# Optimization experiments

Measured on AMD Instinct MI355X. Metric: run time of the kernel, lower is better.

Reference implementation:

```python
import jax, jax.numpy as jnp
import numpy as np

EPS = 1e-06

def _pairwise_giou(pred, target):
    # pred: [B,P,4], target: [B,G,4] -> gious [B,P,G]
    p = pred[:, :, None, :]   # [B,P,1,4]
    t = target[:, None, :, :] # [B,1,G,4]
    pw = jnp.clip(p[..., 2] - p[..., 0] + 1.0, 0.0)
    ph = jnp.clip(p[..., 3] - p[..., 1] + 1.0, 0.0)
    tw = jnp.clip(t[..., 2] - t[..., 0] + 1.0, 0.0)
    th = jnp.clip(t[..., 3] - t[..., 1] + 1.0, 0.0)
    pred_areas = pw * ph
    target_areas = tw * th
    ix1 = jnp.maximum(p[..., 0], t[..., 0])
    iy1 = jnp.maximum(p[..., 1], t[..., 1])
    ix2 = jnp.minimum(p[..., 2], t[..., 2])
    iy2 = jnp.minimum(p[..., 3], t[..., 3])
    iw = jnp.clip(ix2 - ix1 + 1.0, 0.0)
    ih = jnp.clip(iy2 - iy1 + 1.0, 0.0)
    inter = iw * ih
    unions = pred_areas + target_areas - inter
    ious = jnp.maximum(inter / unions, EPS)
    ox1 = jnp.minimum(p[..., 0], t[..., 0])
    oy1 = jnp.minimum(p[..., 1], t[..., 1])
    ox2 = jnp.maximum(p[..., 2], t[..., 2])
    oy2 = jnp.maximum(p[..., 3], t[..., 3])
    ow = jnp.clip(ox2 - ox1 + 1.0, 0.0)
    oh = jnp.clip(oy2 - oy1 + 1.0, 0.0)
    outer = ow * oh
    gious = ious - (outer - unions) / outer
    return jnp.clip(gious, -1.0, 1.0)


def setup_inputs() -> dict:
    key = jax.random.key(0)
    k1, k2, k3, k4, k5 = jax.random.split(key, 5)
    B, P, G = 32, 2048, 512
    IMG = 1024.0
    # gt boxes: [B,G,4] with x1<=x2, y1<=y2
    gxy = jax.random.uniform(k1, (B, G, 2), dtype=jnp.float32) * (IMG - 64.0)
    gwh = jax.random.uniform(k2, (B, G, 2), dtype=jnp.float32) * 64.0 + 1.0
    imgs_box = jnp.concatenate([gxy, gxy + gwh], axis=-1)
    # pred boxes: [B,P,4]
    pxy = jax.random.uniform(k3, (B, P, 2), dtype=jnp.float32) * (IMG - 64.0)
    pwh = jax.random.uniform(k4, (B, P, 2), dtype=jnp.float32) * 64.0 + 1.0
    pre_BOX = jnp.concatenate([pxy, pxy + pwh], axis=-1)
    labels = jax.random.randint(k5, (B,), 0, 10, dtype=jnp.int64 if jax.config.jax_enable_x64 else jnp.int32)
    return {"imgs_box": imgs_box, "pre_BOX": pre_BOX, "labels": labels}


def reference(imgs_box, pre_BOX, labels):
    B = labels.shape[0]
    gious = _pairwise_giou(pre_BOX, imgs_box)      # [B,P,G]
    max_giou = jnp.max(gious, axis=-1)             # [B,P]
    batch_loss = jnp.sum(1.0 - max_giou)
    return batch_loss / B
```

## Files before the change

kernel.cpp:

```cpp
#include <hip/hip_runtime.h>


constexpr int TPL = 8;
constexpr int PPW = 8;
constexpr int NW  = 8;

template <int CTRL>
__device__ __forceinline__ float dppmax(float x) {
    int i = __float_as_int(x);
    int m = __builtin_amdgcn_update_dpp(i, i, CTRL, 0xF, 0xF, false);
    return fmaxf(x, __int_as_float(m));
}

__global__ __launch_bounds__(512, 4) void giou_partial_kernel(
    const float4* __restrict__ tgt,
    const float4* __restrict__ pred,
    float* __restrict__ partial,
    int P, int G)
{
    __shared__ float4 sP[NW * PPW];
    __shared__ float  sOut[NW];

    const int b    = blockIdx.y;
    const int tid  = threadIdx.x;
    const int lane = tid & 63;
    const int wid  = tid >> 6;

    if (tid < NW * PPW) {
        int pi = blockIdx.x * (NW * PPW) + tid;
        float4 v = pred[b * P + min(pi, P - 1)];
        v.z += 1.0f; v.w += 1.0f;
        sP[tid] = v;
    }

    float tx1[TPL], ty1[TPL], tx2[TPL], ty2[TPL];
    #pragma unroll
    for (int j = 0; j < TPL; ++j) {
        float4 t = tgt[b * G + min(j * 64 + lane, G - 1)];
        tx1[j] = t.x; ty1[j] = t.y;
        tx2[j] = t.z + 1.0f; ty2[j] = t.w + 1.0f;
    }
    __syncthreads();

    float acc = 0.0f;

    for (int q = 0; q < PPW; ++q) {
        const int   pidx = blockIdx.x * (NW * PPW) + wid * PPW + q;
        const float4 pbx = sP[wid * PPW + q];
        const float pw = pbx.z - pbx.x;
        const float ph = pbx.w - pbx.y;
        const float pa = pw * ph;

        float numM = 0.0f, denM = 1.0f;

        #pragma unroll
        for (int j = 0; j < TPL; ++j) {
            float tw  = tx2[j] - tx1[j];
            float th  = ty2[j] - ty1[j];
            float ta  = tw * th;
            float iwr = fminf(pbx.z, tx2[j]) - fmaxf(pbx.x, tx1[j]);
            float ihr = fminf(pbx.w, ty2[j]) - fmaxf(pbx.y, ty1[j]);
            float inter = fmaxf(iwr, 0.0f) * fmaxf(ihr, 0.0f);
            float un  = (pa + ta) - inter;
            float ow  = (pw + tw) - iwr;
            float oh  = (ph + th) - ihr;
            float outer = ow * oh;
            float num = __builtin_fmaf(un, un, inter * outer);
            float den = un * outer;
            bool better = num * denM > numM * den;
            numM = better ? num : numM;
            denM = better ? den : denM;
        }

        float gi = numM * __builtin_amdgcn_rcpf(denM);

        gi = dppmax<0x111>(gi);
        gi = dppmax<0x112>(gi);
        gi = dppmax<0x114>(gi);
        gi = dppmax<0x118>(gi);
        gi = dppmax<0x142>(gi);
        gi = dppmax<0x143>(gi);

        if (lane == 63 && pidx < P)
            acc += 2.0f - gi;
    }

    if (lane == 63) sOut[wid] = acc;
    __syncthreads();

    if (tid == 0) {
        float v = 0.0f;
        #pragma unroll
        for (int w = 0; w < NW; ++w) v += sOut[w];
        partial[blockIdx.y * gridDim.x + blockIdx.x] = v;
    }
}

__global__ __launch_bounds__(256) void giou_reduce_kernel(
    const float* __restrict__ partial, float* __restrict__ out, int n, float invB)
{
    const int tid = threadIdx.x;
    float v = 0.0f;
    for (int i = tid; i < n; i += 256) v += partial[i];

    #pragma unroll
    for (int off = 32; off > 0; off >>= 1)
        v += __shfl_down(v, off, 64);

    __shared__ float sW[4];
    const int wid = tid >> 6;
    if ((tid & 63) == 0) sW[wid] = v;
    __syncthreads();
    if (tid == 0)
        out[0] = (sW[0] + sW[1] + sW[2] + sW[3]) * invB;
}

extern "C" void kernel_launch(void* const* d_in, const int* in_sizes, int n_in,
                              void* d_out, int out_size, void* d_ws, size_t ws_size,
                              hipStream_t stream) {
    const float* imgs_box = (const float*)d_in[0];
    const float* pre_box  = (const float*)d_in[1];

    const int B = in_sizes[2];
    const int G = in_sizes[0] / (4 * B);
    const int P = in_sizes[1] / (4 * B);

    float* partial = (float*)d_ws;

    const int pblocks = (P + NW * PPW - 1) / (NW * PPW);
    dim3 grid(pblocks, B);
    giou_partial_kernel<<<grid, 512, 0, stream>>>(
        (const float4*)imgs_box, (const float4*)pre_box, partial, P, G);

    const int n = pblocks * B;
    giou_reduce_kernel<<<1, 256, 0, stream>>>(partial, (float*)d_out, n, 1.0f / (float)B);
}
```

Measured before the change: 34.31 us.

## Bin boxes into spatial grid cells and prune far cells with GIoU bound

Adds a prep kernel that buckets target and predicted boxes into an 8x8 grid of image cells per batch, sorting them by cell and recording per-cell centre extents and maximum sizes and areas. The main kernel loads the sorted targets into shared memory and assigns one thread per predicted box. Each thread evaluates its own cell fully, then skips any other cell whose upper bound on the GIoU ratio cannot beat the current best. This removes most of the all-pairs arithmetic for spatially sparse boxes. In exchange it adds a serial single-block-per-batch prep pass with shared atomics, an extra launch, extra workspace traffic and divergent per-lane work.

```diff
diff --git a/kernel.cpp b/kernel.cpp
--- a/kernel.cpp
+++ b/kernel.cpp
@@ -1,99 +1,174 @@
 #include <hip/hip_runtime.h>
 
 
-constexpr int TPL = 8;
-constexpr int PPW = 8;
-constexpr int NW  = 8;
-
-template <int CTRL>
-__device__ __forceinline__ float dppmax(float x) {
-    int i = __float_as_int(x);
-    int m = __builtin_amdgcn_update_dpp(i, i, CTRL, 0xF, 0xF, false);
-    return fmaxf(x, __int_as_float(m));
-}
-
-__global__ __launch_bounds__(512, 4) void giou_partial_kernel(
-    const float4* __restrict__ tgt,
-    const float4* __restrict__ pred,
-    float* __restrict__ partial,
+constexpr int NCX = 8, NCY = 8, NCELL = NCX * NCY;
+constexpr int GMAXL = 2048;
+
+__device__ __forceinline__ int cell_of(float xc, float yc) {
+    int cx = (int)(xc * (1.0f / 128.0f)); cx = max(0, min(NCX - 1, cx));
+    int cy = (int)(yc * (1.0f / 128.0f)); cy = max(0, min(NCY - 1, cy));
+    return cy * NCX + cx;
+}
+
+__global__ __launch_bounds__(512) void giou_prep_kernel(
+    const float4* __restrict__ tgt, const float4* __restrict__ pred,
+    float4* __restrict__ sortedT, float* __restrict__ sTA,
+    float4* __restrict__ sortedP,
+    int* __restrict__ tstartG, float4* __restrict__ meta0G, float4* __restrict__ meta1G,
+    int* __restrict__ tmpc, int* __restrict__ tmpr,
+    int* __restrict__ pmpc, int* __restrict__ pmpr,
     int P, int G)
 {
-    __shared__ float4 sP[NW * PPW];
-    __shared__ float  sOut[NW];
-
-    const int b    = blockIdx.y;
-    const int tid  = threadIdx.x;
-    const int lane = tid & 63;
-    const int wid  = tid >> 6;
-
-    if (tid < NW * PPW) {
-        int pi = blockIdx.x * (NW * PPW) + tid;
-        float4 v = pred[b * P + min(pi, P - 1)];
-        v.z += 1.0f; v.w += 1.0f;
-        sP[tid] = v;
-    }
-
-    float tx1[TPL], ty1[TPL], tx2[TPL], ty2[TPL];
+    __shared__ int cnt[NCELL], cstart[NCELL + 1];
+    __shared__ int bminx[NCELL], bminy[NCELL], bmaxx[NCELL], bmaxy[NCELL];
+    __shared__ int taM[NCELL], twM[NCELL], thM[NCELL];
+
+    const int b = blockIdx.x, tid = threadIdx.x;
+    if (tid < NCELL) {
+        cnt[tid] = 0;
+        bminx[tid] = 0x7f800000; bminy[tid] = 0x7f800000;
+        bmaxx[tid] = 0; bmaxy[tid] = 0;
+        taM[tid] = 0; twM[tid] = 0; thM[tid] = 0;
+    }
+    __syncthreads();
+
+    for (int g = tid; g < G; g += 512) {
+        float4 t = tgt[b * G + g]; t.z += 1.0f; t.w += 1.0f;
+        float xc = (t.x + t.z) * 0.5f, yc = (t.y + t.w) * 0.5f;
+        int c = cell_of(xc, yc);
+        int r = atomicAdd(&cnt[c], 1);
+        tmpc[b * G + g] = c; tmpr[b * G + g] = r;
+        atomicMin(&bminx[c], __float_as_int(xc));
+        atomicMin(&bminy[c], __float_as_int(yc));
+        atomicMax(&bmaxx[c], __float_as_int(xc));
+        atomicMax(&bmaxy[c], __float_as_int(yc));
+        float tw = t.z - t.x, th = t.w - t.y;
+        atomicMax(&taM[c], __float_as_int(tw * th));
+        atomicMax(&twM[c], __float_as_int(tw * 0.5f));
+        atomicMax(&thM[c], __float_as_int(th * 0.5f));
+    }
+    __syncthreads();
+    if (tid == 0) {
+        int s = 0;
+        for (int c = 0; c < NCELL; ++c) { cstart[c] = s; s += cnt[c]; }
+        cstart[NCELL] = s;
+    }
+    __syncthreads();
+    for (int g = tid; g < G; g += 512) {
+        float4 t = tgt[b * G + g]; t.z += 1.0f; t.w += 1.0f;
+        int pos = cstart[tmpc[b * G + g]] + tmpr[b * G + g];
+        sortedT[b * G + pos] = t;
+        sTA[b * G + pos] = (t.z - t.x) * (t.w - t.y);
+    }
+    if (tid <= NCELL) tstartG[b * (NCELL + 1) + tid] = cstart[tid];
+    if (tid < NCELL) {
+        meta0G[b * NCELL + tid] = make_float4(
+            __int_as_float(bminx[tid]), __int_as_float(bminy[tid]),
+            __int_as_float(bmaxx[tid]), __int_as_float(bmaxy[tid]));
+        meta1G[b * NCELL + tid] = make_float4(
+            __int_as_float(taM[tid]), __int_as_float(twM[tid]),
+            __int_as_float(thM[tid]), 0.0f);
+    }
+
+    __syncthreads();
+    if (tid < NCELL) cnt[tid] = 0;
+    __syncthreads();
+    for (int p = tid; p < P; p += 512) {
+        float4 v = pred[b * P + p]; v.z += 1.0f; v.w += 1.0f;
+        int c = cell_of((v.x + v.z) * 0.5f, (v.y + v.w) * 0.5f);
+        int r = atomicAdd(&cnt[c], 1);
+        pmpc[b * P + p] = c; pmpr[b * P + p] = r;
+    }
+    __syncthreads();
+    if (tid == 0) {
+        int s = 0;
+        for (int c = 0; c < NCELL; ++c) { cstart[c] = s; s += cnt[c]; }
+    }
+    __syncthreads();
+    for (int p = tid; p < P; p += 512) {
+        float4 v = pred[b * P + p]; v.z += 1.0f; v.w += 1.0f;
+        sortedP[b * P + cstart[pmpc[b * P + p]] + pmpr[b * P + p]] = v;
+    }
+}
+
+__global__ __launch_bounds__(256) void giou_main_kernel(
+    const float4* __restrict__ sortedT, const float* __restrict__ sTA,
+    const float4* __restrict__ sortedP,
+    const int* __restrict__ tstartG, const float4* __restrict__ meta0G,
+    const float4* __restrict__ meta1G,
+    float* __restrict__ partial, int P, int G)
+{
+    __shared__ float4 sT4[GMAXL];
+    __shared__ float  sA[GMAXL];
+    __shared__ int    sStart[NCELL + 1];
+    __shared__ float4 sM0[NCELL], sM1[NCELL];
+    __shared__ float  sOut[4];
+
+    const int b = blockIdx.y, tid = threadIdx.x, lane = tid & 63, wid = tid >> 6;
+    const int GL = min(G, GMAXL);
+    for (int i = tid; i < GL; i += 256) { sT4[i] = sortedT[b * G + i]; sA[i] = sTA[b * G + i]; }
+    if (tid <= NCELL) sStart[tid] = min(tstartG[b * (NCELL + 1) + tid], GMAXL);
+    if (tid < NCELL) { sM0[tid] = meta0G[b * NCELL + tid]; sM1[tid] = meta1G[b * NCELL + tid]; }
+    __syncthreads();
+
+    const int slot = blockIdx.x * 256 + tid;
+    const float4 pb = sortedP[b * P + min(slot, P - 1)];
+    const float pw = pb.z - pb.x, ph = pb.w - pb.y, pa = pw * ph;
+    const float pxc = (pb.x + pb.z) * 0.5f, pyc = (pb.y + pb.w) * 0.5f;
+    const int ownc = cell_of(pxc, pyc);
+
+    float numM = 0.0f, denM = 1.0f;
+
+    auto evalT = [&](float4 t, float ta) {
+        float iwr = fminf(pb.z, t.z) - fmaxf(pb.x, t.x);
+        float ihr = fminf(pb.w, t.w) - fmaxf(pb.y, t.y);
+        float inter = fmaxf(iwr, 0.0f) * fmaxf(ihr, 0.0f);
+        float un = (pa + ta) - inter;
+        float outer = ((pw + (t.z - t.x)) - iwr) * ((ph + (t.w - t.y)) - ihr);
+        float num = __builtin_fmaf(un, un, inter * outer);
+        float den = un * outer;
+        bool better = num * denM > numM * den;
+        numM = better ? num : numM;
+        denM = better ? den : denM;
+    };
+
+    for (int i = sStart[ownc]; i < sStart[ownc + 1]; ++i) evalT(sT4[i], sA[i]);
+
+    for (int c = 0; c < NCELL; ++c) {
+        const int s = sStart[c], e = sStart[c + 1];
+        if (e == s) continue;
+        const float4 m0 = sM0[c];
+        const float4 m1 = sM1[c];
+        float dx = fmaxf(0.0f, fmaxf(m0.x - pxc, pxc - m0.z));
+        float dy = fmaxf(0.0f, fmaxf(m0.y - pyc, pyc - m0.w));
+        bool far_x = dx >= __builtin_fmaf(pw, 0.5f, m1.y);
+        bool far_y = dy >= __builtin_fmaf(ph, 0.5f, m1.z);
+        bool act;
+        if (far_x || far_y) {
+            float ub = (pa + m1.x) *
+                       __builtin_amdgcn_rcpf(fmaxf(pw, dx) * fmaxf(ph, dy)) * 1.0002f;
+            act = (ub * denM > numM);
+        } else {
+            act = true;
+        }
+        act = act && (c != ownc);
+        if (__any(act)) {
+            for (int i = s; i < e; ++i) {
+                if (act) evalT(sT4[i], sA[i]);
+            }
+        }
+    }
+
+    for (int g = GMAXL; g < G; ++g) evalT(sortedT[b * G + g], sTA[b * G + g]);
+
+    float m = numM * __builtin_amdgcn_rcpf(denM);
+    float v = (slot < P) ? (2.0f - m) : 0.0f;
     #pragma unroll
-    for (int j = 0; j < TPL; ++j) {
-        float4 t = tgt[b * G + min(j * 64 + lane, G - 1)];
-        tx1[j] = t.x; ty1[j] = t.y;
-        tx2[j] = t.z + 1.0f; ty2[j] = t.w + 1.0f;
-    }
-    __syncthreads();
-
-    float acc = 0.0f;
-
-    for (int q = 0; q < PPW; ++q) {
-        const int   pidx = blockIdx.x * (NW * PPW) + wid * PPW + q;
-        const float4 pbx = sP[wid * PPW + q];
-        const float pw = pbx.z - pbx.x;
-        const float ph = pbx.w - pbx.y;
-        const float pa = pw * ph;
-
-        float numM = 0.0f, denM = 1.0f;
-
-        #pragma unroll
-        for (int j = 0; j < TPL; ++j) {
-            float tw  = tx2[j] - tx1[j];
-            float th  = ty2[j] - ty1[j];
-            float ta  = tw * th;
-            float iwr = fminf(pbx.z, tx2[j]) - fmaxf(pbx.x, tx1[j]);
-            float ihr = fminf(pbx.w, ty2[j]) - fmaxf(pbx.y, ty1[j]);
-            float inter = fmaxf(iwr, 0.0f) * fmaxf(ihr, 0.0f);
-            float un  = (pa + ta) - inter;
-            float ow  = (pw + tw) - iwr;
-            float oh  = (ph + th) - ihr;
-            float outer = ow * oh;
-            float num = __builtin_fmaf(un, un, inter * outer);
-            float den = un * outer;
-            bool better = num * denM > numM * den;
-            numM = better ? num : numM;
-            denM = better ? den : denM;
-        }
-
-        float gi = numM * __builtin_amdgcn_rcpf(denM);
-
-        gi = dppmax<0x111>(gi);
-        gi = dppmax<0x112>(gi);
-        gi = dppmax<0x114>(gi);
-        gi = dppmax<0x118>(gi);
-        gi = dppmax<0x142>(gi);
-        gi = dppmax<0x143>(gi);
-
-        if (lane == 63 && pidx < P)
-            acc += 2.0f - gi;
-    }
-
-    if (lane == 63) sOut[wid] = acc;
-    __syncthreads();
-
-    if (tid == 0) {
-        float v = 0.0f;
-        #pragma unroll
-        for (int w = 0; w < NW; ++w) v += sOut[w];
-        partial[blockIdx.y * gridDim.x + blockIdx.x] = v;
-    }
+    for (int off = 32; off > 0; off >>= 1) v += __shfl_down(v, off, 64);
+    if (lane == 0) sOut[wid] = v;
+    __syncthreads();
+    if (tid == 0)
+        partial[blockIdx.y * gridDim.x + blockIdx.x] = sOut[0] + sOut[1] + sOut[2] + sOut[3];
 }
 
 __global__ __launch_bounds__(256) void giou_reduce_kernel(
@@ -102,17 +177,13 @@
     const int tid = threadIdx.x;
     float v = 0.0f;
     for (int i = tid; i < n; i += 256) v += partial[i];
-
     #pragma unroll
-    for (int off = 32; off > 0; off >>= 1)
-        v += __shfl_down(v, off, 64);
-
+    for (int off = 32; off > 0; off >>= 1) v += __shfl_down(v, off, 64);
     __shared__ float sW[4];
     const int wid = tid >> 6;
     if ((tid & 63) == 0) sW[wid] = v;
     __syncthreads();
-    if (tid == 0)
-        out[0] = (sW[0] + sW[1] + sW[2] + sW[3]) * invB;
+    if (tid == 0) out[0] = (sW[0] + sW[1] + sW[2] + sW[3]) * invB;
 }
 
 extern "C" void kernel_launch(void* const* d_in, const int* in_sizes, int n_in,
@@ -120,18 +191,38 @@
                               hipStream_t stream) {
     const float* imgs_box = (const float*)d_in[0];
     const float* pre_box  = (const float*)d_in[1];
-
     const int B = in_sizes[2];
     const int G = in_sizes[0] / (4 * B);
     const int P = in_sizes[1] / (4 * B);
 
-    float* partial = (float*)d_ws;
-
-    const int pblocks = (P + NW * PPW - 1) / (NW * PPW);
+    char* w = (char*)d_ws;
+    auto alloc = [&](size_t bytes) {
+        char* r = w;
+        w += (bytes + 15) & ~size_t(15);
+        return r;
+    };
+    float4* sortedT = (float4*)alloc((size_t)B * G * 16);
+    float*  sTA     = (float*) alloc((size_t)B * G * 4);
+    float4* sortedP = (float4*)alloc((size_t)B * P * 16);
+    int*    tstartG = (int*)   alloc((size_t)B * (NCELL + 1) * 4);
+    float4* meta0G  = (float4*)alloc((size_t)B * NCELL * 16);
+    float4* meta1G  = (float4*)alloc((size_t)B * NCELL * 16);
+    int*    tmpc    = (int*)   alloc((size_t)B * G * 4);
+    int*    tmpr    = (int*)   alloc((size_t)B * G * 4);
+    int*    pmpc    = (int*)   alloc((size_t)B * P * 4);
+    int*    pmpr    = (int*)   alloc((size_t)B * P * 4);
+    const int pblocks = (P + 255) / 256;
+    float*  partial = (float*) alloc((size_t)pblocks * B * 4);
+
+    giou_prep_kernel<<<B, 512, 0, stream>>>(
+        (const float4*)imgs_box, (const float4*)pre_box,
+        sortedT, sTA, sortedP, tstartG, meta0G, meta1G,
+        tmpc, tmpr, pmpc, pmpr, P, G);
+
     dim3 grid(pblocks, B);
-    giou_partial_kernel<<<grid, 512, 0, stream>>>(
-        (const float4*)imgs_box, (const float4*)pre_box, partial, P, G);
-
-    const int n = pblocks * B;
-    giou_reduce_kernel<<<1, 256, 0, stream>>>(partial, (float*)d_out, n, 1.0f / (float)B);
-}
+    giou_main_kernel<<<grid, 256, 0, stream>>>(
+        sortedT, sTA, sortedP, tstartG, meta0G, meta1G, partial, P, G);
+
+    giou_reduce_kernel<<<1, 256, 0, stream>>>(
+        partial, (float*)d_out, pblocks * B, 1.0f / (float)B);
+}
```

Result: slower. 82.34 us (+140.0%).
